# Kernel optimization log

Measured on AMD Instinct MI355X. Metric: run time of the kernel, lower is better.

The kernel has to match this reference:

```python
import jax, jax.numpy as jnp
import numpy as np
from jax import lax

T, H = 4096, 2048          # tokens, hidden_size
E, K = 64, 8               # n_routed_experts, top_k
I = 512                    # moe_intermediate_size
IS = 512                   # shared intermediate = moe_intermediate_size * n_shared_experts
ROUTED_SCALING = 2.5


def setup_inputs() -> dict:
    key = jax.random.key(0)
    ks = jax.random.split(key, 6)
    return {
        "hidden_states": jax.random.normal(ks[0], (T, H), jnp.float32),
        "gate_w": jax.random.normal(ks[1], (H, E), jnp.float32) * 0.05,
        "w13": jax.random.normal(ks[2], (E, H, 2 * I), jnp.float32) * 0.02,
        "w2": jax.random.normal(ks[3], (E, I, H), jnp.float32) * 0.02,
        "shared_w13": jax.random.normal(ks[4], (H, 2 * IS), jnp.float32) * 0.02,
        "shared_w2": jax.random.normal(ks[5], (IS, H), jnp.float32) * 0.02,
    }


def reference(hidden_states, gate_w, w13, w2, shared_w13, shared_w2):
    # --- router: sigmoid scoring, grouped top-k with 1 group == plain top-k ---
    logits = hidden_states @ gate_w                        # [T, E]
    scores = jax.nn.sigmoid(logits.astype(jnp.float32))
    topk_w, topk_ids = lax.top_k(scores, K)                # [T, K]
    topk_w = topk_w / jnp.sum(topk_w, axis=-1, keepdims=True)  # renormalize

    # --- dispatch: sort token-expert pairs by expert id, grouped GEMM ---
    flat_ids = topk_ids.reshape(-1)                        # [T*K]
    order = jnp.argsort(flat_ids)                          # pairs grouped by expert
    token_idx = order // K                                 # source token of each sorted pair
    x_sorted = hidden_states[token_idx]                    # [T*K, H]
    group_sizes = jnp.bincount(flat_ids, length=E).astype(jnp.int32)

    gu = lax.ragged_dot(x_sorted, w13, group_sizes)        # [T*K, 2I]
    h = jax.nn.silu(gu[:, :I]) * gu[:, I:]                 # SiluAndMul
    out_sorted = lax.ragged_dot(h, w2, group_sizes)        # [T*K, H]

    # --- combine: unsort, weight, sum over top-k ---
    inv = jnp.argsort(order)
    out_pairs = out_sorted[inv].reshape(T, K, H)
    routed = jnp.sum(out_pairs * topk_w[..., None].astype(out_pairs.dtype), axis=1)

    # --- shared expert MLP ---
    sg = hidden_states @ shared_w13                        # [T, 2*IS]
    shared = (jax.nn.silu(sg[:, :IS]) * sg[:, IS:]) @ shared_w2

    return routed * ROUTED_SCALING + shared
```

## Files before the change

kernel.cpp:

```cpp
#include <hip/hip_runtime.h>
#include <hip/hip_bf16.h>

#define T_TOK 4096
#define HD    2048
#define NE    64
#define TOPK  8
#define IMID  512
#define N13   1024
#define NPAIR (T_TOK*TOPK)
#define NROWS (NPAIR + T_TOK)
#define MAXT2 208
#define RSCALE 2.5f

typedef __attribute__((ext_vector_type(8)))  __bf16 bf16x8;
typedef __attribute__((ext_vector_type(4)))  float  f32x4;

__global__ void init_small(int* __restrict__ counts, int* __restrict__ curs) {
  int tid = threadIdx.x;
  if (tid < NE + 1) { counts[tid] = 0; curs[tid] = 0; }
}
__global__ __launch_bounds__(256) void zero_out_kernel(float4* __restrict__ out4) {
  out4[blockIdx.x * 256 + threadIdx.x] = float4{0.f, 0.f, 0.f, 0.f};
}

__global__ __launch_bounds__(256) void cvt_kernel(const float4* __restrict__ hs4,
                                                  bf16x8* __restrict__ hb8) {
  int gid = blockIdx.x * 256 + threadIdx.x;
  float4 a = hs4[2 * gid], b = hs4[2 * gid + 1];
  bf16x8 v = { (__bf16)a.x, (__bf16)a.y, (__bf16)a.z, (__bf16)a.w,
               (__bf16)b.x, (__bf16)b.y, (__bf16)b.z, (__bf16)b.w };
  hb8[gid] = v;
}

__global__ __launch_bounds__(256) void logits_kernel(const float* __restrict__ hs,
                                                     const float* __restrict__ gw,
                                                     float* __restrict__ logits) {
  __shared__ float hsm[64][16];
  __shared__ float gwm[64][64];
  int tid = threadIdx.x;
  int tb = blockIdx.x * 16;
  int tok = tid >> 4, e4 = (tid & 15) * 4;
  float acc[4] = {0.f, 0.f, 0.f, 0.f};
  for (int c = 0; c < 32; ++c) {
    int kb = c * 64;
    {
      int t16 = tid & 15, kq = tid >> 4;
      float4 f = *(const float4*)&hs[(size_t)(tb + t16) * HD + kb + kq * 4];
      hsm[kq * 4 + 0][t16] = f.x; hsm[kq * 4 + 1][t16] = f.y;
      hsm[kq * 4 + 2][t16] = f.z; hsm[kq * 4 + 3][t16] = f.w;
#pragma unroll
      for (int it = 0; it < 4; ++it) {
        int q = tid + it * 256;
        int gr = q >> 4, gc = (q & 15) * 4;
        *(float4*)&gwm[gr][gc] = *(const float4*)&gw[(size_t)(kb + gr) * NE + gc];
      }
    }
    __syncthreads();
#pragma unroll 8
    for (int k = 0; k < 64; ++k) {
      float h = hsm[k][tok];
      float4 g = *(const float4*)&gwm[k][e4];
      acc[0] += h * g.x; acc[1] += h * g.y; acc[2] += h * g.z; acc[3] += h * g.w;
    }
    __syncthreads();
  }
#pragma unroll
  for (int j = 0; j < 4; ++j) logits[(size_t)(tb + tok) * NE + e4 + j] = acc[j];
}

__global__ __launch_bounds__(256) void top8_kernel(const float* __restrict__ logits,
                                                   int* __restrict__ topk_id,
                                                   float* __restrict__ pair_w,
                                                   int* __restrict__ counts) {
  int lane = threadIdx.x & 63;
  int t = blockIdx.x * 4 + (threadIdx.x >> 6);
  float v = logits[(size_t)t * NE + lane];
  float s = 1.f / (1.f + __expf(-v));
  float cur = s, ssum = 0.f;
  int myid = 0; float myw = 0.f;
  for (int k = 0; k < TOPK; ++k) {
    float bv = cur; int bi = lane;
#pragma unroll
    for (int off = 32; off >= 1; off >>= 1) {
      float ov = __shfl_xor(bv, off);
      int   oi = __shfl_xor(bi, off);
      if (ov > bv || (ov == bv && oi < bi)) { bv = ov; bi = oi; }
    }
    ssum += bv;
    if (lane == k) { myid = bi; myw = bv; }
    if (lane == bi) cur = -1.f;
  }
  if (lane < TOPK) {
    topk_id[(size_t)t * TOPK + lane] = myid;
    pair_w[(size_t)t * TOPK + lane] = myw / ssum * RSCALE;
    atomicAdd(&counts[myid], 1);
  }
}

__global__ void scan_kernel(const int* __restrict__ counts, int* __restrict__ offs,
                            int2* __restrict__ tiles) {
  __shared__ int cnt[65], pref[66], tp[66];
  int tid = threadIdx.x;
  if (tid < 64) cnt[tid] = counts[tid];
  if (tid == 64) cnt[64] = T_TOK;
  __syncthreads();
  if (tid == 0) {
    int o = 0, t = 0;
    for (int e = 0; e <= 64; ++e) {
      pref[e] = o; tp[e] = t;
      o += cnt[e]; t += (cnt[e] + 255) >> 8;
    }
    pref[65] = o; tp[65] = t;
  }
  __syncthreads();
  if (tid <= 64) {
    offs[tid] = pref[tid];
    int c = cnt[tid], base = pref[tid], tb = tp[tid];
    int nt = (c + 255) >> 8;
    for (int i = 0; i < nt; ++i) {
      int rr = c - i * 256; if (rr > 256) rr = 256;
      tiles[tb + i] = make_int2(base + i * 256, (tid << 16) | rr);
    }
  }
  __syncthreads();
  for (int i = tp[65] + tid; i < MAXT2; i += 128) tiles[i] = make_int2(0, 0);
}

__global__ __launch_bounds__(256) void scatter_kernel(const int* __restrict__ topk_id,
                                                      const float* __restrict__ pair_w,
                                                      const int* __restrict__ offs,
                                                      int* __restrict__ curs,
                                                      int* __restrict__ row_token,
                                                      float* __restrict__ row_w,
                                                      int* __restrict__ inv8) {
  int p = blockIdx.x * 256 + threadIdx.x;
  int dst, t; float w;
  if (p < NPAIR) {
    t = p >> 3; int e = topk_id[p]; w = pair_w[p];
    dst = offs[e] + atomicAdd(&curs[e], 1);
    inv8[p] = dst;
  } else {
    t = p - NPAIR; w = 1.0f;
    dst = NPAIR + t;
  }
  row_token[dst] = t;
  row_w[dst] = w;
}

__device__ __forceinline__ int swz(int row, int kbyte) {
  return row * 128 + (kbyte ^ ((row & 7) << 4));
}
__device__ __forceinline__ void glds16(const void* g, void* l) {
  __builtin_amdgcn_global_load_lds((const __attribute__((address_space(1))) void*)g,
                                   (__attribute__((address_space(3))) void*)l, 16, 0, 0);
}
__device__ __forceinline__ void store_bx8(__bf16* Bs, int col, int kbyte, const float* p) {
  bf16x8 v = { (__bf16)p[0], (__bf16)p[1], (__bf16)p[2], (__bf16)p[3],
               (__bf16)p[4], (__bf16)p[5], (__bf16)p[6], (__bf16)p[7] };
  *(bf16x8*)&Bs[swz(col, kbyte) >> 1] = v;
}

#define G1STEP(S, ACUR, ANX2, BGc, BUc, BGn, BUn, RL, RS)                                  \
  {                                                                                        \
    if ((S) + 2 < 32) {                                                                    \
      const float* Bn_ = Bp0 + (size_t)((S) + 2) * 64 * N13;                               \
      _Pragma("unroll") for (int r = 0; r < 8; ++r) RL[r] = Bn_[(size_t)r * N13];          \
      __builtin_amdgcn_sched_barrier(0);                                                   \
      _Pragma("unroll") for (int i = 0; i < 2; ++i)                                        \
        glds16(Abase[i] + ((S) + 2) * 64, (ANX2) + wv * 1024 + i * 512);                   \
    }                                                                                      \
    __builtin_amdgcn_sched_barrier(0);                                                     \
    __builtin_amdgcn_s_setprio(1);                                                         \
    _Pragma("unroll") for (int kk = 0; kk < 2; ++kk) {                                     \
      int koff = kk * 64 + lq * 16;                                                        \
      bf16x8 a[2], bg[2], bu[2];                                                           \
      _Pragma("unroll") for (int i = 0; i < 2; ++i)                                        \
        a[i] = *(const bf16x8*)&(ACUR)[swz(wrow * 32 + i * 16 + l15, koff) >> 1];          \
      _Pragma("unroll") for (int j = 0; j < 2; ++j) {                                      \
        bg[j] = *(const bf16x8*)&(BGc)[swz(wc * 32 + j * 16 + l15, koff) >> 1];            \
        bu[j] = *(const bf16x8*)&(BUc)[swz(wc * 32 + j * 16 + l15, koff) >> 1];            \
      }                                                                                    \
      _Pragma("unroll") for (int i = 0; i < 2; ++i)                                        \
        _Pragma("unroll") for (int j = 0; j < 2; ++j) {                                    \
          accg[i][j] = __builtin_amdgcn_mfma_f32_16x16x32_bf16(a[i], bg[j], accg[i][j], 0, 0, 0); \
          accu[i][j] = __builtin_amdgcn_mfma_f32_16x16x32_bf16(a[i], bu[j], accu[i][j], 0, 0, 0); \
        }                                                                                  \
    }                                                                                      \
    __builtin_amdgcn_s_setprio(0);                                                         \
    if ((S) + 1 < 32) {                                                                    \
      __bf16* Bmy_ = bm ? (BUn) : (BGn);                                                   \
      store_bx8(Bmy_, bcol, bkq * 16, RS);                                                 \
    }                                                                                      \
    if ((S) + 2 < 32) asm volatile("s_waitcnt vmcnt(10) lgkmcnt(0)" ::: "memory");         \
    else              asm volatile("s_waitcnt vmcnt(0) lgkmcnt(0)"  ::: "memory");         \
    __builtin_amdgcn_s_barrier();                                                          \
    __builtin_amdgcn_sched_barrier(0);                                                     \
  }

__global__ __launch_bounds__(1024, 4) void gemm1_kernel(const __bf16* __restrict__ hidden_bf,
                                                        const float* __restrict__ w13,
                                                        const float* __restrict__ sw13,
                                                        const int* __restrict__ row_token,
                                                        const int2* __restrict__ tiles,
                                                        __bf16* __restrict__ hbuf) {
  int2 td = tiles[blockIdx.y];
  int rows = td.y & 0xFFFF;
  if (rows == 0) return;
  int e = td.y >> 16, row0 = td.x;
  const float* W = (e < NE) ? (w13 + (size_t)e * (HD * N13)) : sw13;
  int n0 = blockIdx.x * 64;

  __shared__ __bf16 As0[256 * 64], As1[256 * 64], As2[256 * 64];
  __shared__ __bf16 Bgs[2][64 * 64];
  __shared__ __bf16 Bus[2][64 * 64];

  int tid = threadIdx.x;
  int lane = tid & 63, wv = tid >> 6;
  int wrow = wv >> 1, wc = wv & 1;
  int l15 = lane & 15, lq = lane >> 4;

  int kswz = (((lane & 7) ^ ((lane >> 3) & 7)) << 3);
  const __bf16* Abase[2];
#pragma unroll
  for (int i = 0; i < 2; ++i) {
    int grow = row0 + wv * 16 + i * 8 + (lane >> 3);
    if (grow >= NROWS) grow = NROWS - 1;
    Abase[i] = hidden_bf + (size_t)row_token[grow] * HD + kswz;
  }
  int bm = tid >> 9, bcol = tid & 63, bkq = (tid >> 6) & 7;
  const float* Bp0 = W + (size_t)(bkq * 8) * N13 + (bm ? 512 + n0 : n0) + bcol;

  float pA[8], pB[8];
#pragma unroll
  for (int r = 0; r < 8; ++r) pA[r] = Bp0[(size_t)r * N13];
  __builtin_amdgcn_sched_barrier(0);
#pragma unroll
  for (int i = 0; i < 2; ++i) glds16(Abase[i], As0 + wv * 1024 + i * 512);
  __builtin_amdgcn_sched_barrier(0);
  {
    const float* B1 = Bp0 + (size_t)64 * N13;
#pragma unroll
    for (int r = 0; r < 8; ++r) pB[r] = B1[(size_t)r * N13];
  }
  __builtin_amdgcn_sched_barrier(0);
#pragma unroll
  for (int i = 0; i < 2; ++i) glds16(Abase[i] + 64, As1 + wv * 1024 + i * 512);
  __builtin_amdgcn_sched_barrier(0);
  {
    __bf16* Bmy = bm ? Bus[0] : Bgs[0];
    store_bx8(Bmy, bcol, bkq * 16, pA);
  }
  asm volatile("s_waitcnt vmcnt(10) lgkmcnt(0)" ::: "memory");
  __builtin_amdgcn_s_barrier();
  __builtin_amdgcn_sched_barrier(0);

  f32x4 accg[2][2], accu[2][2];
#pragma unroll
  for (int i = 0; i < 2; ++i)
#pragma unroll
    for (int j = 0; j < 2; ++j) { accg[i][j] = (f32x4)(0.f); accu[i][j] = (f32x4)(0.f); }

  __bf16 *Ac = As0, *A1 = As1, *A2 = As2;
  for (int s = 0; s < 32; s += 2) {
    G1STEP(s,     Ac, A2, Bgs[0], Bus[0], Bgs[1], Bus[1], pA, pB);
    { __bf16* t = Ac; Ac = A1; A1 = A2; A2 = t; }
    G1STEP(s + 1, Ac, A2, Bgs[1], Bus[1], Bgs[0], Bus[0], pB, pA);
    { __bf16* t = Ac; Ac = A1; A1 = A2; A2 = t; }
  }
#pragma unroll
  for (int mi = 0; mi < 2; ++mi) {
#pragma unroll
    for (int r = 0; r < 4; ++r) {
      int rl = wrow * 32 + mi * 16 + lq * 4 + r;
      if (rl < rows) {
        size_t hrow = (size_t)(row0 + rl) * IMID;
#pragma unroll
        for (int j = 0; j < 2; ++j) {
          float g = accg[mi][j][r], u = accu[mi][j][r];
          float hv = g * u / (1.f + __expf(-g));
          hbuf[hrow + n0 + wc * 32 + j * 16 + l15] = (__bf16)hv;
        }
      }
    }
  }
}

#define G2STEP(S, ACUR, ANX2, Bc, Bn, RL, RS)                                              \
  {                                                                                        \
    if ((S) + 2 < 8) {                                                                     \
      const float* Bn_ = Bp0 + (size_t)((S) + 2) * 64 * HD;                                \
      _Pragma("unroll") for (int r = 0; r < 8; ++r) RL[r] = Bn_[(size_t)r * HD];           \
      __builtin_amdgcn_sched_barrier(0);                                                   \
      _Pragma("unroll") for (int i = 0; i < 2; ++i)                                        \
        glds16(Abase[i] + ((S) + 2) * 64, (ANX2) + wv * 1024 + i * 512);                   \
    }                                                                                      \
    __builtin_amdgcn_sched_barrier(0);                                                     \
    __builtin_amdgcn_s_setprio(1);                                                         \
    _Pragma("unroll") for (int kk = 0; kk < 2; ++kk) {                                     \
      int koff = kk * 64 + lq * 16;                                                        \
      bf16x8 a[4], b[2];                                                                   \
      _Pragma("unroll") for (int i = 0; i < 4; ++i)                                        \
        a[i] = *(const bf16x8*)&(ACUR)[swz(wr * 64 + i * 16 + l15, koff) >> 1];            \
      _Pragma("unroll") for (int j = 0; j < 2; ++j)                                        \
        b[j] = *(const bf16x8*)&(Bc)[swz(wc * 32 + j * 16 + l15, koff) >> 1];              \
      _Pragma("unroll") for (int i = 0; i < 4; ++i)                                        \
        _Pragma("unroll") for (int j = 0; j < 2; ++j)                                      \
          acc[i][j] = __builtin_amdgcn_mfma_f32_16x16x32_bf16(a[i], b[j], acc[i][j], 0, 0, 0); \
    }                                                                                      \
    __builtin_amdgcn_s_setprio(0);                                                         \
    if ((S) + 1 < 8) store_bx8((Bn), bcol, bkq * 16, RS);                                  \
    if ((S) + 2 < 8) asm volatile("s_waitcnt vmcnt(10) lgkmcnt(0)" ::: "memory");          \
    else             asm volatile("s_waitcnt vmcnt(0) lgkmcnt(0)"  ::: "memory");          \
    __builtin_amdgcn_s_barrier();                                                          \
    __builtin_amdgcn_sched_barrier(0);                                                     \
  }

template<int MODE>
__global__ __launch_bounds__(1024, 4) void gemm2_kernel(const __bf16* __restrict__ hbuf,
                                                        const float* __restrict__ w2,
                                                        const float* __restrict__ sw2,
                                                        const int* __restrict__ row_token,
                                                        const float* __restrict__ row_w,
                                                        const int2* __restrict__ tiles,
                                                        float* __restrict__ dst) {
  int2 td = tiles[blockIdx.y];
  int rows = td.y & 0xFFFF;
  if (rows == 0) return;
  int e = td.y >> 16, row0 = td.x;
  const float* W = (e < NE) ? (w2 + (size_t)e * (IMID * HD)) : sw2;
  int n0 = blockIdx.x * 128;

  __shared__ __bf16 As0[256 * 64], As1[256 * 64], As2[256 * 64];
  __shared__ __bf16 Bs[2][128 * 64];

  int tid = threadIdx.x;
  int lane = tid & 63, wv = tid >> 6;
  int wr = wv >> 2, wc = wv & 3;
  int l15 = lane & 15, lq = lane >> 4;

  int kswz = (((lane & 7) ^ ((lane >> 3) & 7)) << 3);
  const __bf16* Abase[2];
#pragma unroll
  for (int i = 0; i < 2; ++i) {
    int grow = row0 + wv * 16 + i * 8 + (lane >> 3);
    if (grow >= NROWS) grow = NROWS - 1;
    Abase[i] = hbuf + (size_t)grow * IMID + kswz;
  }
  int bcol = tid & 127, bkq = tid >> 7;
  const float* Bp0 = W + (size_t)(bkq * 8) * HD + n0 + bcol;

  float pA[8], pB[8];
#pragma unroll
  for (int r = 0; r < 8; ++r) pA[r] = Bp0[(size_t)r * HD];
  __builtin_amdgcn_sched_barrier(0);
#pragma unroll
  for (int i = 0; i < 2; ++i) glds16(Abase[i], As0 + wv * 1024 + i * 512);
  __builtin_amdgcn_sched_barrier(0);
  {
    const float* B1 = Bp0 + (size_t)64 * HD;
#pragma unroll
    for (int r = 0; r < 8; ++r) pB[r] = B1[(size_t)r * HD];
  }
  __builtin_amdgcn_sched_barrier(0);
#pragma unroll
  for (int i = 0; i < 2; ++i) glds16(Abase[i] + 64, As1 + wv * 1024 + i * 512);
  __builtin_amdgcn_sched_barrier(0);
  store_bx8(Bs[0], bcol, bkq * 16, pA);
  asm volatile("s_waitcnt vmcnt(10) lgkmcnt(0)" ::: "memory");
  __builtin_amdgcn_s_barrier();
  __builtin_amdgcn_sched_barrier(0);

  f32x4 acc[4][2];
#pragma unroll
  for (int i = 0; i < 4; ++i)
#pragma unroll
    for (int j = 0; j < 2; ++j) acc[i][j] = (f32x4)(0.f);

  __bf16 *Ac = As0, *A1 = As1, *A2 = As2;
  for (int s = 0; s < 8; s += 2) {
    G2STEP(s,     Ac, A2, Bs[0], Bs[1], pA, pB);
    { __bf16* t = Ac; Ac = A1; A1 = A2; A2 = t; }
    G2STEP(s + 1, Ac, A2, Bs[1], Bs[0], pB, pA);
    { __bf16* t = Ac; Ac = A1; A1 = A2; A2 = t; }
  }
#pragma unroll
  for (int i = 0; i < 4; ++i) {
#pragma unroll
    for (int r = 0; r < 4; ++r) {
      int rl = wr * 64 + i * 16 + lq * 4 + r;
      if (rl < rows) {
        int gr = row0 + rl;
        float wgt = row_w[gr];
        if (MODE == 1) {
          float* prow = dst + (size_t)gr * HD + n0 + wc * 32;
#pragma unroll
          for (int j = 0; j < 2; ++j)
            prow[j * 16 + l15] = acc[i][j][r] * wgt;
        } else {
          int tok = row_token[gr];
          float* orow = dst + (size_t)tok * HD + n0 + wc * 32;
#pragma unroll
          for (int j = 0; j < 2; ++j)
            atomicAdd(&orow[j * 16 + l15], acc[i][j][r] * wgt);
        }
      }
    }
  }
}

__global__ __launch_bounds__(256) void combine_kernel(const float* __restrict__ pairout,
                                                      const int* __restrict__ inv8,
                                                      float* __restrict__ out) {
  int t = blockIdx.x;
  int c = threadIdx.x * 8;
  float s0 = 0.f, s1 = 0.f, s2 = 0.f, s3 = 0.f, s4 = 0.f, s5 = 0.f, s6 = 0.f, s7 = 0.f;
#pragma unroll
  for (int k = 0; k < 8; ++k) {
    const float4* pr = (const float4*)(pairout + (size_t)inv8[t * 8 + k] * HD + c);
    float4 a = pr[0], b = pr[1];
    s0 += a.x; s1 += a.y; s2 += a.z; s3 += a.w;
    s4 += b.x; s5 += b.y; s6 += b.z; s7 += b.w;
  }
  {
    const float4* pr = (const float4*)(pairout + (size_t)(NPAIR + t) * HD + c);
    float4 a = pr[0], b = pr[1];
    s0 += a.x; s1 += a.y; s2 += a.z; s3 += a.w;
    s4 += b.x; s5 += b.y; s6 += b.z; s7 += b.w;
  }
  float4* o = (float4*)(out + (size_t)t * HD + c);
  o[0] = float4{s0, s1, s2, s3};
  o[1] = float4{s4, s5, s6, s7};
}

extern "C" void kernel_launch(void* const* d_in, const int* in_sizes, int n_in,
                              void* d_out, int out_size, void* d_ws, size_t ws_size,
                              hipStream_t stream) {
  const float* hidden = (const float*)d_in[0];
  const float* gate_w = (const float*)d_in[1];
  const float* w13    = (const float*)d_in[2];
  const float* w2     = (const float*)d_in[3];
  const float* sw13   = (const float*)d_in[4];
  const float* sw2    = (const float*)d_in[5];
  float* out = (float*)d_out;

  char* ws = (char*)d_ws;
  size_t off = 0;
  __bf16* hbuf      = (__bf16*)(ws + off); off += (size_t)NROWS * IMID * 2;
  __bf16* hidden_bf = (__bf16*)(ws + off); off += (size_t)T_TOK * HD * 2;
  float* logits  = (float*)(ws + off);  off += (size_t)T_TOK * NE * 4;
  int*   topk_id = (int*)(ws + off);    off += (size_t)NPAIR * 4;
  float* pair_w  = (float*)(ws + off);  off += (size_t)NPAIR * 4;
  int*   row_tok = (int*)(ws + off);    off += (size_t)NROWS * 4;
  float* row_w   = (float*)(ws + off);  off += (size_t)NROWS * 4;
  int*   inv8    = (int*)(ws + off);    off += (size_t)NPAIR * 4;
  int*   counts  = (int*)(ws + off);    off += 512;
  int*   curs    = (int*)(ws + off);    off += 512;
  int*   offs    = (int*)(ws + off);    off += 512;
  int2*  tiles   = (int2*)(ws + off);   off += MAXT2 * 8;
  off = (off + 255) & ~(size_t)255;
  float* pairout = (float*)(ws + off);
  size_t need = off + (size_t)NROWS * HD * 4;
  bool rows_path = (ws_size >= need);

  init_small<<<1, 256, 0, stream>>>(counts, curs);
  if (!rows_path)
    zero_out_kernel<<<T_TOK * HD / 4 / 256, 256, 0, stream>>>((float4*)out);
  cvt_kernel<<<T_TOK * HD / 8 / 256, 256, 0, stream>>>((const float4*)hidden, (bf16x8*)hidden_bf);
  logits_kernel<<<T_TOK / 16, 256, 0, stream>>>(hidden, gate_w, logits);
  top8_kernel<<<T_TOK / 4, 256, 0, stream>>>(logits, topk_id, pair_w, counts);
  scan_kernel<<<1, 128, 0, stream>>>(counts, offs, tiles);
  scatter_kernel<<<NROWS / 256, 256, 0, stream>>>(topk_id, pair_w, offs, curs,
                                                  row_tok, row_w, inv8);
  gemm1_kernel<<<dim3(8, MAXT2), 1024, 0, stream>>>(hidden_bf, w13, sw13, row_tok, tiles, hbuf);
  if (rows_path) {
    gemm2_kernel<1><<<dim3(16, MAXT2), 1024, 0, stream>>>(hbuf, w2, sw2, row_tok, row_w,
                                                          tiles, pairout);
    combine_kernel<<<T_TOK, 256, 0, stream>>>(pairout, inv8, out);
  } else {
    gemm2_kernel<0><<<dim3(16, MAXT2), 1024, 0, stream>>>(hbuf, w2, sw2, row_tok, row_w,
                                                          tiles, out);
  }
}
```

Baseline: 798.8 us.

## Halve expert M-tile to 128 rows with 512-thread GEMM blocks

Routed-expert tiles shrink from 256 to 128 rows, so the tile count bound rises and each GEMM block runs 8 waves instead of 16. Each thread now prefetches 16 fp32 weight values per stage instead of 8, and gemm2's wave layout is reshaped to 2x4 MFMA subtiles per wave. This targets padding waste in partially filled expert tiles and lets more blocks fit per CU through smaller LDS. The cost is that weight tiles are reloaded from global memory twice as often per row, plus higher register pressure from the larger prefetch buffers.

```diff
diff --git a/kernel.cpp b/kernel.cpp
--- a/kernel.cpp
+++ b/kernel.cpp
@@ -9,7 +9,7 @@
 #define N13   1024
 #define NPAIR (T_TOK*TOPK)
 #define NROWS (NPAIR + T_TOK)
-#define MAXT2 208
+#define MAXT1 352
 #define RSCALE 2.5f
 
 typedef __attribute__((ext_vector_type(8)))  __bf16 bf16x8;
@@ -108,7 +108,7 @@
     int o = 0, t = 0;
     for (int e = 0; e <= 64; ++e) {
       pref[e] = o; tp[e] = t;
-      o += cnt[e]; t += (cnt[e] + 255) >> 8;
+      o += cnt[e]; t += (cnt[e] + 127) >> 7;
     }
     pref[65] = o; tp[65] = t;
   }
@@ -116,14 +116,14 @@
   if (tid <= 64) {
     offs[tid] = pref[tid];
     int c = cnt[tid], base = pref[tid], tb = tp[tid];
-    int nt = (c + 255) >> 8;
+    int nt = (c + 127) >> 7;
     for (int i = 0; i < nt; ++i) {
-      int rr = c - i * 256; if (rr > 256) rr = 256;
-      tiles[tb + i] = make_int2(base + i * 256, (tid << 16) | rr);
+      int rr = c - i * 128; if (rr > 128) rr = 128;
+      tiles[tb + i] = make_int2(base + i * 128, (tid << 16) | rr);
     }
   }
   __syncthreads();
-  for (int i = tp[65] + tid; i < MAXT2; i += 128) tiles[i] = make_int2(0, 0);
+  for (int i = tp[65] + tid; i < MAXT1; i += 128) tiles[i] = make_int2(0, 0);
 }
 
 __global__ __launch_bounds__(256) void scatter_kernel(const int* __restrict__ topk_id,
@@ -160,14 +160,14 @@
   *(bf16x8*)&Bs[swz(col, kbyte) >> 1] = v;
 }
 
-#define G1STEP(S, ACUR, ANX2, BGc, BUc, BGn, BUn, RL, RS)                                  \
+#define G1STEP(S, Acur, Anx2, BGc, BUc, BGn, BUn, RL, RS)                                  \
   {                                                                                        \
     if ((S) + 2 < 32) {                                                                    \
       const float* Bn_ = Bp0 + (size_t)((S) + 2) * 64 * N13;                               \
-      _Pragma("unroll") for (int r = 0; r < 8; ++r) RL[r] = Bn_[(size_t)r * N13];          \
+      _Pragma("unroll") for (int r = 0; r < 16; ++r) RL[r] = Bn_[(size_t)r * N13];         \
       __builtin_amdgcn_sched_barrier(0);                                                   \
       _Pragma("unroll") for (int i = 0; i < 2; ++i)                                        \
-        glds16(Abase[i] + ((S) + 2) * 64, (ANX2) + wv * 1024 + i * 512);                   \
+        glds16(Abase[i] + ((S) + 2) * 64, (Anx2) + wv * 1024 + i * 512);                   \
     }                                                                                      \
     __builtin_amdgcn_sched_barrier(0);                                                     \
     __builtin_amdgcn_s_setprio(1);                                                         \
@@ -175,7 +175,7 @@
       int koff = kk * 64 + lq * 16;                                                        \
       bf16x8 a[2], bg[2], bu[2];                                                           \
       _Pragma("unroll") for (int i = 0; i < 2; ++i)                                        \
-        a[i] = *(const bf16x8*)&(ACUR)[swz(wrow * 32 + i * 16 + l15, koff) >> 1];          \
+        a[i] = *(const bf16x8*)&(Acur)[swz(wrow * 32 + i * 16 + l15, koff) >> 1];          \
       _Pragma("unroll") for (int j = 0; j < 2; ++j) {                                      \
         bg[j] = *(const bf16x8*)&(BGc)[swz(wc * 32 + j * 16 + l15, koff) >> 1];            \
         bu[j] = *(const bf16x8*)&(BUc)[swz(wc * 32 + j * 16 + l15, koff) >> 1];            \
@@ -189,20 +189,21 @@
     __builtin_amdgcn_s_setprio(0);                                                         \
     if ((S) + 1 < 32) {                                                                    \
       __bf16* Bmy_ = bm ? (BUn) : (BGn);                                                   \
-      store_bx8(Bmy_, bcol, bkq * 16, RS);                                                 \
-    }                                                                                      \
-    if ((S) + 2 < 32) asm volatile("s_waitcnt vmcnt(10) lgkmcnt(0)" ::: "memory");         \
+      store_bx8(Bmy_, bcol, bkq * 32, RS);                                                 \
+      store_bx8(Bmy_, bcol, bkq * 32 + 16, RS + 8);                                        \
+    }                                                                                      \
+    if ((S) + 2 < 32) asm volatile("s_waitcnt vmcnt(18) lgkmcnt(0)" ::: "memory");         \
     else              asm volatile("s_waitcnt vmcnt(0) lgkmcnt(0)"  ::: "memory");         \
     __builtin_amdgcn_s_barrier();                                                          \
     __builtin_amdgcn_sched_barrier(0);                                                     \
   }
 
-__global__ __launch_bounds__(1024, 4) void gemm1_kernel(const __bf16* __restrict__ hidden_bf,
-                                                        const float* __restrict__ w13,
-                                                        const float* __restrict__ sw13,
-                                                        const int* __restrict__ row_token,
-                                                        const int2* __restrict__ tiles,
-                                                        __bf16* __restrict__ hbuf) {
+__global__ __launch_bounds__(512, 4) void gemm1_kernel(const __bf16* __restrict__ hidden_bf,
+                                                       const float* __restrict__ w13,
+                                                       const float* __restrict__ sw13,
+                                                       const int* __restrict__ row_token,
+                                                       const int2* __restrict__ tiles,
+                                                       __bf16* __restrict__ hbuf) {
   int2 td = tiles[blockIdx.y];
   int rows = td.y & 0xFFFF;
   if (rows == 0) return;
@@ -210,7 +211,7 @@
   const float* W = (e < NE) ? (w13 + (size_t)e * (HD * N13)) : sw13;
   int n0 = blockIdx.x * 64;
 
-  __shared__ __bf16 As0[256 * 64], As1[256 * 64], As2[256 * 64];
+  __shared__ __bf16 As0[128 * 64], As1[128 * 64], As2[128 * 64];
   __shared__ __bf16 Bgs[2][64 * 64];
   __shared__ __bf16 Bus[2][64 * 64];
 
@@ -227,12 +228,12 @@
     if (grow >= NROWS) grow = NROWS - 1;
     Abase[i] = hidden_bf + (size_t)row_token[grow] * HD + kswz;
   }
-  int bm = tid >> 9, bcol = tid & 63, bkq = (tid >> 6) & 7;
-  const float* Bp0 = W + (size_t)(bkq * 8) * N13 + (bm ? 512 + n0 : n0) + bcol;
-
-  float pA[8], pB[8];
-#pragma unroll
-  for (int r = 0; r < 8; ++r) pA[r] = Bp0[(size_t)r * N13];
+  int bm = tid >> 8, bcol = tid & 63, bkq = (tid >> 6) & 3;
+  const float* Bp0 = W + (size_t)(bkq * 16) * N13 + (bm ? 512 + n0 : n0) + bcol;
+
+  float pA[16], pB[16];
+#pragma unroll
+  for (int r = 0; r < 16; ++r) pA[r] = Bp0[(size_t)r * N13];
   __builtin_amdgcn_sched_barrier(0);
 #pragma unroll
   for (int i = 0; i < 2; ++i) glds16(Abase[i], As0 + wv * 1024 + i * 512);
@@ -240,7 +241,7 @@
   {
     const float* B1 = Bp0 + (size_t)64 * N13;
 #pragma unroll
-    for (int r = 0; r < 8; ++r) pB[r] = B1[(size_t)r * N13];
+    for (int r = 0; r < 16; ++r) pB[r] = B1[(size_t)r * N13];
   }
   __builtin_amdgcn_sched_barrier(0);
 #pragma unroll
@@ -248,9 +249,10 @@
   __builtin_amdgcn_sched_barrier(0);
   {
     __bf16* Bmy = bm ? Bus[0] : Bgs[0];
-    store_bx8(Bmy, bcol, bkq * 16, pA);
-  }
-  asm volatile("s_waitcnt vmcnt(10) lgkmcnt(0)" ::: "memory");
+    store_bx8(Bmy, bcol, bkq * 32, pA);
+    store_bx8(Bmy, bcol, bkq * 32 + 16, pA + 8);
+  }
+  asm volatile("s_waitcnt vmcnt(18) lgkmcnt(0)" ::: "memory");
   __builtin_amdgcn_s_barrier();
   __builtin_amdgcn_sched_barrier(0);
 
@@ -285,44 +287,47 @@
   }
 }
 
-#define G2STEP(S, ACUR, ANX2, Bc, Bn, RL, RS)                                              \
+#define G2STEP(S, Acur, Anx2, Bc, Bn, RL, RS)                                              \
   {                                                                                        \
     if ((S) + 2 < 8) {                                                                     \
       const float* Bn_ = Bp0 + (size_t)((S) + 2) * 64 * HD;                                \
-      _Pragma("unroll") for (int r = 0; r < 8; ++r) RL[r] = Bn_[(size_t)r * HD];           \
+      _Pragma("unroll") for (int r = 0; r < 16; ++r) RL[r] = Bn_[(size_t)r * HD];          \
       __builtin_amdgcn_sched_barrier(0);                                                   \
       _Pragma("unroll") for (int i = 0; i < 2; ++i)                                        \
-        glds16(Abase[i] + ((S) + 2) * 64, (ANX2) + wv * 1024 + i * 512);                   \
+        glds16(Abase[i] + ((S) + 2) * 64, (Anx2) + wv * 1024 + i * 512);                   \
     }                                                                                      \
     __builtin_amdgcn_sched_barrier(0);                                                     \
     __builtin_amdgcn_s_setprio(1);                                                         \
     _Pragma("unroll") for (int kk = 0; kk < 2; ++kk) {                                     \
       int koff = kk * 64 + lq * 16;                                                        \
-      bf16x8 a[4], b[2];                                                                   \
-      _Pragma("unroll") for (int i = 0; i < 4; ++i)                                        \
-        a[i] = *(const bf16x8*)&(ACUR)[swz(wr * 64 + i * 16 + l15, koff) >> 1];            \
-      _Pragma("unroll") for (int j = 0; j < 2; ++j)                                        \
-        b[j] = *(const bf16x8*)&(Bc)[swz(wc * 32 + j * 16 + l15, koff) >> 1];              \
-      _Pragma("unroll") for (int i = 0; i < 4; ++i)                                        \
-        _Pragma("unroll") for (int j = 0; j < 2; ++j)                                      \
+      bf16x8 a[2], b[4];                                                                   \
+      _Pragma("unroll") for (int i = 0; i < 2; ++i)                                        \
+        a[i] = *(const bf16x8*)&(Acur)[swz(wrow * 32 + i * 16 + l15, koff) >> 1];          \
+      _Pragma("unroll") for (int j = 0; j < 4; ++j)                                        \
+        b[j] = *(const bf16x8*)&(Bc)[swz(wc * 64 + j * 16 + l15, koff) >> 1];              \
+      _Pragma("unroll") for (int i = 0; i < 2; ++i)                                        \
+        _Pragma("unroll") for (int j = 0; j < 4; ++j)                                      \
           acc[i][j] = __builtin_amdgcn_mfma_f32_16x16x32_bf16(a[i], b[j], acc[i][j], 0, 0, 0); \
     }                                                                                      \
     __builtin_amdgcn_s_setprio(0);                                                         \
-    if ((S) + 1 < 8) store_bx8((Bn), bcol, bkq * 16, RS);                                  \
-    if ((S) + 2 < 8) asm volatile("s_waitcnt vmcnt(10) lgkmcnt(0)" ::: "memory");          \
+    if ((S) + 1 < 8) {                                                                     \
+      store_bx8((Bn), bcol, bkq * 32, RS);                                                 \
+      store_bx8((Bn), bcol, bkq * 32 + 16, RS + 8);                                        \
+    }                                                                                      \
+    if ((S) + 2 < 8) asm volatile("s_waitcnt vmcnt(18) lgkmcnt(0)" ::: "memory");          \
     else             asm volatile("s_waitcnt vmcnt(0) lgkmcnt(0)"  ::: "memory");          \
     __builtin_amdgcn_s_barrier();                                                          \
     __builtin_amdgcn_sched_barrier(0);                                                     \
   }
 
 template<int MODE>
-__global__ __launch_bounds__(1024, 4) void gemm2_kernel(const __bf16* __restrict__ hbuf,
-                                                        const float* __restrict__ w2,
-                                                        const float* __restrict__ sw2,
-                                                        const int* __restrict__ row_token,
-                                                        const float* __restrict__ row_w,
-                                                        const int2* __restrict__ tiles,
-                                                        float* __restrict__ dst) {
+__global__ __launch_bounds__(512, 4) void gemm2_kernel(const __bf16* __restrict__ hbuf,
+                                                       const float* __restrict__ w2,
+                                                       const float* __restrict__ sw2,
+                                                       const int* __restrict__ row_token,
+                                                       const float* __restrict__ row_w,
+                                                       const int2* __restrict__ tiles,
+                                                       float* __restrict__ dst) {
   int2 td = tiles[blockIdx.y];
   int rows = td.y & 0xFFFF;
   if (rows == 0) return;
@@ -330,12 +335,12 @@
   const float* W = (e < NE) ? (w2 + (size_t)e * (IMID * HD)) : sw2;
   int n0 = blockIdx.x * 128;
 
-  __shared__ __bf16 As0[256 * 64], As1[256 * 64], As2[256 * 64];
+  __shared__ __bf16 As0[128 * 64], As1[128 * 64], As2[128 * 64];
   __shared__ __bf16 Bs[2][128 * 64];
 
   int tid = threadIdx.x;
   int lane = tid & 63, wv = tid >> 6;
-  int wr = wv >> 2, wc = wv & 3;
+  int wrow = wv >> 1, wc = wv & 1;
   int l15 = lane & 15, lq = lane >> 4;
 
   int kswz = (((lane & 7) ^ ((lane >> 3) & 7)) << 3);
@@ -347,11 +352,11 @@
     Abase[i] = hbuf + (size_t)grow * IMID + kswz;
   }
   int bcol = tid & 127, bkq = tid >> 7;
-  const float* Bp0 = W + (size_t)(bkq * 8) * HD + n0 + bcol;
-
-  float pA[8], pB[8];
-#pragma unroll
-  for (int r = 0; r < 8; ++r) pA[r] = Bp0[(size_t)r * HD];
+  const float* Bp0 = W + (size_t)(bkq * 16) * HD + n0 + bcol;
+
+  float pA[16], pB[16];
+#pragma unroll
+  for (int r = 0; r < 16; ++r) pA[r] = Bp0[(size_t)r * HD];
   __builtin_amdgcn_sched_barrier(0);
 #pragma unroll
   for (int i = 0; i < 2; ++i) glds16(Abase[i], As0 + wv * 1024 + i * 512);
@@ -359,22 +364,23 @@
   {
     const float* B1 = Bp0 + (size_t)64 * HD;
 #pragma unroll
-    for (int r = 0; r < 8; ++r) pB[r] = B1[(size_t)r * HD];
+    for (int r = 0; r < 16; ++r) pB[r] = B1[(size_t)r * HD];
   }
   __builtin_amdgcn_sched_barrier(0);
 #pragma unroll
   for (int i = 0; i < 2; ++i) glds16(Abase[i] + 64, As1 + wv * 1024 + i * 512);
   __builtin_amdgcn_sched_barrier(0);
-  store_bx8(Bs[0], bcol, bkq * 16, pA);
-  asm volatile("s_waitcnt vmcnt(10) lgkmcnt(0)" ::: "memory");
+  store_bx8(Bs[0], bcol, bkq * 32, pA);
+  store_bx8(Bs[0], bcol, bkq * 32 + 16, pA + 8);
+  asm volatile("s_waitcnt vmcnt(18) lgkmcnt(0)" ::: "memory");
   __builtin_amdgcn_s_barrier();
   __builtin_amdgcn_sched_barrier(0);
 
-  f32x4 acc[4][2];
-#pragma unroll
-  for (int i = 0; i < 4; ++i)
-#pragma unroll
-    for (int j = 0; j < 2; ++j) acc[i][j] = (f32x4)(0.f);
+  f32x4 acc[2][4];
+#pragma unroll
+  for (int i = 0; i < 2; ++i)
+#pragma unroll
+    for (int j = 0; j < 4; ++j) acc[i][j] = (f32x4)(0.f);
 
   __bf16 *Ac = As0, *A1 = As1, *A2 = As2;
   for (int s = 0; s < 8; s += 2) {
@@ -384,24 +390,24 @@
     { __bf16* t = Ac; Ac = A1; A1 = A2; A2 = t; }
   }
 #pragma unroll
-  for (int i = 0; i < 4; ++i) {
+  for (int mi = 0; mi < 2; ++mi) {
 #pragma unroll
     for (int r = 0; r < 4; ++r) {
-      int rl = wr * 64 + i * 16 + lq * 4 + r;
+      int rl = wrow * 32 + mi * 16 + lq * 4 + r;
       if (rl < rows) {
         int gr = row0 + rl;
         float wgt = row_w[gr];
         if (MODE == 1) {
-          float* prow = dst + (size_t)gr * HD + n0 + wc * 32;
-#pragma unroll
-          for (int j = 0; j < 2; ++j)
-            prow[j * 16 + l15] = acc[i][j][r] * wgt;
+          float* prow = dst + (size_t)gr * HD + n0 + wc * 64;
+#pragma unroll
+          for (int j = 0; j < 4; ++j)
+            prow[j * 16 + l15] = acc[mi][j][r] * wgt;
         } else {
           int tok = row_token[gr];
-          float* orow = dst + (size_t)tok * HD + n0 + wc * 32;
-#pragma unroll
-          for (int j = 0; j < 2; ++j)
-            atomicAdd(&orow[j * 16 + l15], acc[i][j][r] * wgt);
+          float* orow = dst + (size_t)tok * HD + n0 + wc * 64;
+#pragma unroll
+          for (int j = 0; j < 4; ++j)
+            atomicAdd(&orow[j * 16 + l15], acc[mi][j][r] * wgt);
         }
       }
     }
@@ -456,7 +462,7 @@
   int*   counts  = (int*)(ws + off);    off += 512;
   int*   curs    = (int*)(ws + off);    off += 512;
   int*   offs    = (int*)(ws + off);    off += 512;
-  int2*  tiles   = (int2*)(ws + off);   off += MAXT2 * 8;
+  int2*  tiles   = (int2*)(ws + off);   off += MAXT1 * 8;
   off = (off + 255) & ~(size_t)255;
   float* pairout = (float*)(ws + off);
   size_t need = off + (size_t)NROWS * HD * 4;
@@ -471,13 +477,13 @@
   scan_kernel<<<1, 128, 0, stream>>>(counts, offs, tiles);
   scatter_kernel<<<NROWS / 256, 256, 0, stream>>>(topk_id, pair_w, offs, curs,
                                                   row_tok, row_w, inv8);
-  gemm1_kernel<<<dim3(8, MAXT2), 1024, 0, stream>>>(hidden_bf, w13, sw13, row_tok, tiles, hbuf);
+  gemm1_kernel<<<dim3(8, MAXT1), 512, 0, stream>>>(hidden_bf, w13, sw13, row_tok, tiles, hbuf);
   if (rows_path) {
-    gemm2_kernel<1><<<dim3(16, MAXT2), 1024, 0, stream>>>(hbuf, w2, sw2, row_tok, row_w,
-                                                          tiles, pairout);
+    gemm2_kernel<1><<<dim3(16, MAXT1), 512, 0, stream>>>(hbuf, w2, sw2, row_tok, row_w,
+                                                         tiles, pairout);
     combine_kernel<<<T_TOK, 256, 0, stream>>>(pairout, inv8, out);
   } else {
-    gemm2_kernel<0><<<dim3(16, MAXT2), 1024, 0, stream>>>(hbuf, w2, sw2, row_tok, row_w,
-                                                          tiles, out);
-  }
-}
+    gemm2_kernel<0><<<dim3(16, MAXT1), 512, 0, stream>>>(hbuf, w2, sw2, row_tok, row_w,
+                                                         tiles, out);
+  }
+}
```

New measurement: 773.4 us. 1.03x faster.
